# Performance work log

Measured on AMD Instinct MI355X. Metric: run time of the kernel, lower is better.

## Reference

```python
import jax, jax.numpy as jnp
import numpy as np


def _conv(x, w, b=None, stride=1, pad=0):
    y = jax.lax.conv_general_dilated(x, w, (stride, stride), [(pad, pad), (pad, pad)],
                                     dimension_numbers=('NCHW', 'OIHW', 'NCHW'))
    if b is not None:
        y = y + b[None, :, None, None]
    return y


def _slice3d(grid, guide):
    # Trilinear grid_sample, align_corners=False, zero padding.
    # grid: (N, C=12, D=8, GH, GW); guide: (N,1,H,W) in [-1,1]
    N, C, D, GH, GW = grid.shape
    H, W = guide.shape[2], guide.shape[3]
    xs = 2.0 * jnp.arange(W, dtype=grid.dtype) / max(W - 1, 1) - 1.0
    ys = 2.0 * jnp.arange(H, dtype=grid.dtype) / max(H - 1, 1) - 1.0
    gx = ((xs + 1.0) * GW - 1.0) * 0.5               # (W,)
    gy = ((ys + 1.0) * GH - 1.0) * 0.5               # (H,)
    gz = ((guide[:, 0] + 1.0) * D - 1.0) * 0.5       # (N,H,W)
    x0f = jnp.floor(gx); y0f = jnp.floor(gy); z0f = jnp.floor(gz)
    fx = gx - x0f; fy = gy - y0f; fz = gz - z0f
    x0 = x0f.astype(jnp.int32); y0 = y0f.astype(jnp.int32); z0 = z0f.astype(jnp.int32)
    gf = grid.reshape(N, C, D * GH * GW)

    def corner(zi, yi, xi, wz, wy, wx):
        mask = ((zi >= 0) & (zi < D)) & ((yi >= 0) & (yi < GH))[None, :, None] & ((xi >= 0) & (xi < GW))[None, None, :]
        zc = jnp.clip(zi, 0, D - 1); yc = jnp.clip(yi, 0, GH - 1); xc = jnp.clip(xi, 0, GW - 1)
        flat = zc * (GH * GW) + yc[None, :, None] * GW + xc[None, None, :]   # (N,H,W)
        v = jnp.take_along_axis(gf, flat.reshape(N, 1, H * W), axis=2).reshape(N, C, H, W)
        w = (wz * wy[None, :, None] * wx[None, None, :]) * mask.astype(grid.dtype)  # (N,H,W)
        return v * w[:, None]

    out = jnp.zeros((N, C, H, W), grid.dtype)
    for dz in (0, 1):
        for dy in (0, 1):
            for dx in (0, 1):
                out = out + corner(z0 + dz, y0 + dy, x0 + dx,
                                   fz if dz else 1.0 - fz,
                                   fy if dy else 1.0 - fy,
                                   fx if dx else 1.0 - fx)
    return out


def setup_inputs() -> dict:
    key = jax.random.key(0)
    ks = jax.random.split(key, 40)
    def w(i, shape):
        return jax.random.normal(ks[i], shape, jnp.float32) * 0.05
    return {
        'low_res': jax.random.uniform(ks[0], (4, 3, 256, 256), jnp.float32),
        'full_res': jax.random.uniform(ks[1], (4, 1, 1024, 1024), jnp.float32),
        'w0': w(2, (8, 3, 3, 3)), 'b0': w(3, (8,)),
        'w1': w(4, (16, 8, 3, 3)), 'b1': w(5, (16,)),
        'w2': w(6, (32, 16, 3, 3)), 'b2': w(7, (32,)),
        'w3': w(8, (64, 32, 3, 3)), 'b3': w(9, (64,)),
        'wl0': w(10, (64, 64, 3, 3)), 'bl0': w(11, (64,)),
        'wl1': w(12, (64, 64, 3, 3)),
        'wg1': w(13, (128, 64, 3, 3)), 'bg1': w(14, (128,)),
        'wg2': w(15, (256, 128, 3, 3)), 'bg2': w(16, (256,)),
        'wf1': w(17, (256, 448, 1, 1)), 'bf1': w(18, (256,)),
        'wf2': w(19, (128, 256, 1, 1)), 'bf2': w(20, (128,)),
        'wf3': w(21, (64, 128, 1, 1)), 'bf3': w(22, (64,)),
        'wlin': w(23, (96, 64, 1, 1)), 'blin': w(24, (96,)),
        'wgd1': w(25, (16, 1, 3, 3)), 'bgd1': w(26, (16,)),
        'wgd2': w(27, (1, 16, 1, 1)), 'bgd2': w(28, (1,)),
        'wau1': w(29, (16, 1, 1, 1)), 'bau1': w(30, (16,)),
        'wau2': w(31, (1, 16, 1, 1)), 'bau2': w(32, (1,)),
        'wav1': w(33, (16, 1, 1, 1)), 'bav1': w(34, (16,)),
        'wav2': w(35, (1, 16, 1, 1)), 'bav2': w(36, (1,)),
    }


def reference(low_res, full_res, w0, b0, w1, b1, w2, b2, w3, b3, wl0, bl0, wl1,
              wg1, bg1, wg2, bg2, wf1, bf1, wf2, bf2, wf3, bf3, wlin, blin,
              wgd1, bgd1, wgd2, bgd2, wau1, bau1, wau2, bau2, wav1, bav1, wav2, bav2):
    relu = jax.nn.relu
    N = low_res.shape[0]
    H, W = full_res.shape[2], full_res.shape[3]
    fake = jax.image.resize(low_res, (N, 3, H, W), 'bilinear')
    # splat stack: 4 stride-2 convs
    x = relu(_conv(low_res, w0, b0, 2, 1))
    x = relu(_conv(x, w1, b1, 2, 1))
    x = relu(_conv(x, w2, b2, 2, 1))
    splat = relu(_conv(x, w3, b3, 2, 1))                 # (N,64,16,16)
    local = _conv(relu(_conv(splat, wl0, bl0, 1, 1)), wl1, None, 1, 1)
    # global branch
    a0 = splat.mean(axis=(2, 3), keepdims=True)
    x1 = relu(_conv(splat, wg1, bg1, 2, 1))
    a1 = x1.mean(axis=(2, 3), keepdims=True)
    x2 = relu(_conv(x1, wg2, bg2, 2, 1))
    a2 = x2.mean(axis=(2, 3), keepdims=True)
    a = jnp.concatenate([a0, a1, a2], axis=1)            # (N,448,1,1)
    a = relu(_conv(a, wf1, bf1))
    a = relu(_conv(a, wf2, bf2))
    glob = relu(_conv(a, wf3, bf3))                      # (N,64,1,1)
    fused = relu(glob + local)
    fused = _conv(fused, wlin, blin)                     # (N,96,16,16)
    grid = fused.reshape(N, 12, 8, fused.shape[2], fused.shape[3])
    guidemap = jnp.tanh(_conv(relu(_conv(full_res, wgd1, bgd1, 1, 1)), wgd2, bgd2))
    coeff = _slice3d(grid, guidemap)                     # (N,12,H,W)
    Y = full_res * coeff[:, 3:4] + coeff[:, 0:3].sum(axis=1, keepdims=True)
    U0 = full_res * coeff[:, 7:8] + coeff[:, 4:7].sum(axis=1, keepdims=True)
    V0 = full_res * coeff[:, 11:12] + coeff[:, 8:11].sum(axis=1, keepdims=True)
    U = jnp.tanh(_conv(relu(_conv(U0, wau1, bau1)), wau2, bau2)) + fake[:, 1:2]
    V = jnp.tanh(_conv(relu(_conv(V0, wav1, bav1)), wav2, bav2)) + fake[:, 2:3]
    return jnp.concatenate([Y, U, V], axis=1)
```

## Files before the change

kernel.cpp:

```cpp
#include <hip/hip_runtime.h>
#include <math.h>


typedef float v2f __attribute__((ext_vector_type(2)));

__device__ __forceinline__ float tanh_fast(float x) {
    float e = __expf(2.0f * x);
    return 1.0f - 2.0f / (e + 1.0f);
}

template<int CIN, int COUT, int HIN, int WIN, int HOUT, int WOUT>
__global__ __launch_bounds__(256) void conv_s2_small(
    const float* __restrict__ in, const float* __restrict__ w,
    const float* __restrict__ b, float* __restrict__ out)
{
    int idx = blockIdx.x * 256 + threadIdx.x;
    int wo = idx % WOUT; int t = idx / WOUT;
    int ho = t % HOUT; t /= HOUT;
    int co = t % COUT; int n = t / COUT;
    float acc = b[co];
    int hi0 = ho * 2 - 1, wi0 = wo * 2 - 1;
    const float* wp = w + (size_t)co * CIN * 9;
    #pragma unroll
    for (int ci = 0; ci < CIN; ++ci) {
        const float* ip = in + ((size_t)(n * CIN + ci)) * HIN * WIN;
        const float* wc = wp + ci * 9;
        #pragma unroll
        for (int kh = 0; kh < 3; ++kh) {
            int hi = hi0 + kh;
            if ((unsigned)hi >= (unsigned)HIN) continue;
            const float* row = ip + hi * WIN;
            #pragma unroll
            for (int kw = 0; kw < 3; ++kw) {
                int wi = wi0 + kw;
                if ((unsigned)wi >= (unsigned)WIN) continue;
                acc = fmaf(wc[kh * 3 + kw], row[wi], acc);
            }
        }
    }
    out[idx] = fmaxf(acc, 0.0f);
}

template<int CIN, int PARTS, int STRIDE, bool RELU, bool HASB,
         int COUT, int HIN, int WIN, int HOUT, int WOUT>
__device__ __forceinline__ void conv_p_dev(
    const float* __restrict__ in, const float* __restrict__ w,
    const float* __restrict__ b, float* __restrict__ out,
    int tb, float* red)
{
    constexpr int CPT = CIN / PARTS;
    constexpr int OPB = 256 / PARTS;
    int part = threadIdx.x / OPB;
    int oidx = threadIdx.x % OPB;
    int o = tb * OPB + oidx;
    int wo = o % WOUT; int t = o / WOUT;
    int ho = t % HOUT; t /= HOUT;
    int co = t % COUT; int n = t / COUT;
    int hi0 = ho * STRIDE - 1, wi0 = wo * STRIDE - 1;
    const float* wp = w + ((size_t)co * CIN + part * CPT) * 9;
    const float* ip = in + ((size_t)n * CIN + part * CPT) * HIN * WIN;
    float acc = 0.0f;
    #pragma unroll
    for (int ci = 0; ci < CPT; ++ci) {
        const float* ic = ip + (size_t)ci * HIN * WIN;
        const float* wc = wp + ci * 9;
        #pragma unroll
        for (int kh = 0; kh < 3; ++kh) {
            int hi = hi0 + kh;
            if ((unsigned)hi >= (unsigned)HIN) continue;
            const float* row = ic + hi * WIN;
            #pragma unroll
            for (int kw = 0; kw < 3; ++kw) {
                int wi = wi0 + kw;
                if ((unsigned)wi >= (unsigned)WIN) continue;
                acc = fmaf(wc[kh * 3 + kw], row[wi], acc);
            }
        }
    }
    red[threadIdx.x] = acc;
    __syncthreads();
    if (part == 0) {
        float s = acc;
        #pragma unroll
        for (int p = 1; p < PARTS; ++p) s += red[p * OPB + oidx];
        if (HASB) s += b[co];
        if (RELU) s = fmaxf(s, 0.0f);
        out[o] = s;
    }
}

__global__ __launch_bounds__(256) void conv2_k(
    const float* __restrict__ in, const float* __restrict__ w,
    const float* __restrict__ b, float* __restrict__ out)
{
    __shared__ float red[256];
    conv_p_dev<16, 4, 2, true, true, 32, 64, 64, 32, 32>(in, w, b, out, blockIdx.x, red);
}

__global__ __launch_bounds__(256) void conv3_k(
    const float* __restrict__ in, const float* __restrict__ w,
    const float* __restrict__ b, float* __restrict__ out)
{
    __shared__ float red[256];
    conv_p_dev<32, 8, 2, true, true, 64, 32, 32, 16, 16>(in, w, b, out, blockIdx.x, red);
}

__global__ __launch_bounds__(256) void k5_l0_g1(
    const float* __restrict__ splat,
    const float* __restrict__ wl0, const float* __restrict__ bl0, float* __restrict__ l0o,
    const float* __restrict__ wg1, const float* __restrict__ bg1, float* __restrict__ x1)
{
    __shared__ float red[256];
    int bid = blockIdx.x;
    if (bid < 4096)
        conv_p_dev<64, 16, 1, true, true, 64, 16, 16, 16, 16>(splat, wl0, bl0, l0o, bid, red);
    else
        conv_p_dev<64, 16, 2, true, true, 128, 16, 16, 8, 8>(splat, wg1, bg1, x1, bid - 4096, red);
}

__global__ __launch_bounds__(256) void k6_l1_g2_means(
    const float* __restrict__ l0o, const float* __restrict__ wl1, float* __restrict__ localb,
    const float* __restrict__ x1, const float* __restrict__ wg2,
    const float* __restrict__ bg2, float* __restrict__ x2,
    const float* __restrict__ splat, float* __restrict__ avec)
{
    __shared__ float red[256];
    int bid = blockIdx.x;
    if (bid < 4096) {
        conv_p_dev<64, 16, 1, false, false, 64, 16, 16, 16, 16>(l0o, wl1, nullptr, localb, bid, red);
    } else if (bid < 5120) {
        conv_p_dev<128, 16, 2, true, true, 256, 8, 8, 4, 4>(x1, wg2, bg2, x2, bid - 4096, red);
    } else if (bid < 5184) {
        int wid = (bid - 5120) * 4 + (threadIdx.x >> 6);
        int lane = threadIdx.x & 63;
        int n = wid >> 6, c = wid & 63;
        const float* p = splat + ((size_t)(n * 64 + c)) * 256;
        float s = p[lane] + p[lane + 64] + p[lane + 128] + p[lane + 192];
        #pragma unroll
        for (int off = 32; off; off >>= 1) s += __shfl_down(s, off, 64);
        if (lane == 0) avec[n * 448 + c] = s * (1.0f / 256.0f);
    } else {
        int wid = (bid - 5184) * 4 + (threadIdx.x >> 6);
        int lane = threadIdx.x & 63;
        int n = wid >> 7, c = wid & 127;
        const float* p = x1 + ((size_t)(n * 128 + c)) * 64;
        float s = p[lane];
        #pragma unroll
        for (int off = 32; off; off >>= 1) s += __shfl_down(s, off, 64);
        if (lane == 0) avec[n * 448 + 64 + c] = s * (1.0f / 64.0f);
    }
}

__global__ __launch_bounds__(256) void fc_k(
    const float* __restrict__ avec, const float* __restrict__ x2,
    const float* __restrict__ wf1, const float* __restrict__ bf1,
    const float* __restrict__ wf2, const float* __restrict__ bf2,
    const float* __restrict__ wf3, const float* __restrict__ bf3,
    float* __restrict__ glob)
{
    __shared__ float a[448];
    __shared__ float h1[256];
    __shared__ float h2[128];
    int n = blockIdx.x, t = threadIdx.x;
    if (t < 192) a[t] = avec[n * 448 + t];
    {
        const float* p = x2 + ((size_t)(n * 256 + t)) * 16;
        float s = 0.0f;
        #pragma unroll
        for (int i = 0; i < 16; ++i) s += p[i];
        a[192 + t] = s * (1.0f / 16.0f);
    }
    __syncthreads();
    {
        float a0 = 0, a1 = 0, a2 = 0, a3 = 0;
        const float* wp = wf1 + (size_t)t * 448;
        for (int i = 0; i < 448; i += 4) {
            a0 = fmaf(wp[i], a[i], a0); a1 = fmaf(wp[i + 1], a[i + 1], a1);
            a2 = fmaf(wp[i + 2], a[i + 2], a2); a3 = fmaf(wp[i + 3], a[i + 3], a3);
        }
        float s = a0 + a1 + a2 + a3 + bf1[t];
        __syncthreads();
        h1[t] = fmaxf(s, 0.0f);
    }
    __syncthreads();
    if (t < 128) {
        float a0 = 0, a1 = 0, a2 = 0, a3 = 0;
        const float* wp = wf2 + (size_t)t * 256;
        for (int i = 0; i < 256; i += 4) {
            a0 = fmaf(wp[i], h1[i], a0); a1 = fmaf(wp[i + 1], h1[i + 1], a1);
            a2 = fmaf(wp[i + 2], h1[i + 2], a2); a3 = fmaf(wp[i + 3], h1[i + 3], a3);
        }
        h2[t] = fmaxf(a0 + a1 + a2 + a3 + bf2[t], 0.0f);
    }
    __syncthreads();
    if (t < 64) {
        float a0 = 0, a1 = 0, a2 = 0, a3 = 0;
        const float* wp = wf3 + (size_t)t * 128;
        for (int i = 0; i < 128; i += 4) {
            a0 = fmaf(wp[i], h2[i], a0); a1 = fmaf(wp[i + 1], h2[i + 1], a1);
            a2 = fmaf(wp[i + 2], h2[i + 2], a2); a3 = fmaf(wp[i + 3], h2[i + 3], a3);
        }
        glob[n * 64 + t] = fmaxf(a0 + a1 + a2 + a3 + bf3[t], 0.0f);
    }
}

__global__ __launch_bounds__(256) void fuse_grid(
    const float* __restrict__ glob, const float* __restrict__ local,
    const float* __restrict__ wlin, const float* __restrict__ blin,
    float* __restrict__ grid)
{
    int idx = blockIdx.x * 256 + threadIdx.x;
    int p = idx & 255; int k = (idx >> 8) % 96; int n = idx / (96 * 256);
    float acc = blin[k];
    const float* wp = wlin + k * 64;
    const float* gl = glob + n * 64;
    const float* lo = local + (size_t)n * 64 * 256 + p;
    #pragma unroll 8
    for (int c = 0; c < 64; ++c)
        acc = fmaf(wp[c], fmaxf(gl[c] + lo[c * 256], 0.0f), acc);
    int ch = k >> 3; int z = k & 7;
    grid[(((size_t)(n * 8 + z)) * 256 + p) * 12 + ch] = acc;
}

__global__ __launch_bounds__(256) void hdr_out_v3(
    const float* __restrict__ full, const float* __restrict__ low,
    const float* __restrict__ grid,
    const float* __restrict__ wgd1, const float* __restrict__ bgd1,
    const float* __restrict__ wgd2, const float* __restrict__ bgd2,
    const float* __restrict__ wau1, const float* __restrict__ bau1,
    const float* __restrict__ wau2, const float* __restrict__ bau2,
    const float* __restrict__ wav1, const float* __restrict__ bav1,
    const float* __restrict__ wav2, const float* __restrict__ bav2,
    float* __restrict__ out)
{
    int tid = blockIdx.x * 256 + threadIdx.x;
    int x0 = (tid & 255) << 2;
    int y = (tid >> 8) & 1023;
    int n = tid >> 18;
    const float* fp = full + ((size_t)n << 20);

    float v[3][6];
    #pragma unroll
    for (int r = 0; r < 3; ++r) {
        int yy = y + r - 1;
        bool okr = (unsigned)yy < 1024u;
        const float* row = fp + (size_t)yy * 1024;
        if (okr) {
            float4 m = *(const float4*)(row + x0);
            v[r][1] = m.x; v[r][2] = m.y; v[r][3] = m.z; v[r][4] = m.w;
            v[r][0] = (x0 > 0) ? row[x0 - 1] : 0.0f;
            v[r][5] = (x0 < 1020) ? row[x0 + 4] : 0.0f;
        } else {
            #pragma unroll
            for (int j = 0; j < 6; ++j) v[r][j] = 0.0f;
        }
    }

    float gacc[4];
    float bb = bgd2[0];
    #pragma unroll
    for (int px = 0; px < 4; ++px) gacc[px] = bb;
    #pragma unroll
    for (int k = 0; k < 16; ++k) {
        const float* wk = wgd1 + k * 9;
        float q0 = wk[0], q1 = wk[1], q2 = wk[2];
        float q3 = wk[3], q4 = wk[4], q5 = wk[5];
        float q6 = wk[6], q7 = wk[7], q8 = wk[8];
        float bk = bgd1[k], wo = wgd2[k];
        #pragma unroll
        for (int px = 0; px < 4; ++px) {
            float h = bk;
            h = fmaf(q0, v[0][px], h); h = fmaf(q1, v[0][px + 1], h); h = fmaf(q2, v[0][px + 2], h);
            h = fmaf(q3, v[1][px], h); h = fmaf(q4, v[1][px + 1], h); h = fmaf(q5, v[1][px + 2], h);
            h = fmaf(q6, v[2][px], h); h = fmaf(q7, v[2][px + 1], h); h = fmaf(q8, v[2][px + 2], h);
            gacc[px] = fmaf(wo, fmaxf(h, 0.0f), gacc[px]);
        }
    }

    float gyc = (y * (32.0f / 1023.0f) - 1.0f) * 0.5f;
    float y0f = floorf(gyc); float fy = gyc - y0f; int iy = (int)y0f;
    float wy0 = (iy >= 0 && iy < 16) ? (1.0f - fy) : 0.0f;
    float wy1 = (iy + 1 < 16) ? fy : 0.0f;
    int yi0 = min(max(iy, 0), 15), yi1 = min(iy + 1, 15);

    float sy = (y + 0.5f) * 0.25f - 0.5f;
    float syf = floorf(sy); float fyl = sy - syf;
    int jy0 = max((int)syf, 0), jy1 = min((int)syf + 1, 255);
    int jc = x0 >> 2;
    int c0 = max(jc - 1, 0), c2 = min(jc + 1, 255);
    const float* lr1 = low + ((size_t)(n * 3 + 1)) * 65536;
    const float* lr2 = low + ((size_t)(n * 3 + 2)) * 65536;
    float ua = lr1[jy0 * 256 + c0] + fyl * (lr1[jy1 * 256 + c0] - lr1[jy0 * 256 + c0]);
    float ub = lr1[jy0 * 256 + jc] + fyl * (lr1[jy1 * 256 + jc] - lr1[jy0 * 256 + jc]);
    float uc = lr1[jy0 * 256 + c2] + fyl * (lr1[jy1 * 256 + c2] - lr1[jy0 * 256 + c2]);
    float va = lr2[jy0 * 256 + c0] + fyl * (lr2[jy1 * 256 + c0] - lr2[jy0 * 256 + c0]);
    float vb = lr2[jy0 * 256 + jc] + fyl * (lr2[jy1 * 256 + jc] - lr2[jy0 * 256 + jc]);
    float vc = lr2[jy0 * 256 + c2] + fyl * (lr2[jy1 * 256 + c2] - lr2[jy0 * 256 + c2]);
    const float cfx[4] = {0.625f, 0.875f, 0.125f, 0.375f};

    const float* gbase = grid + (size_t)n * 24576;
    float Yo[4], Uo[4], Vo[4];

    #pragma unroll
    for (int px = 0; px < 4; ++px) {
        int x = x0 + px;
        float g = tanh_fast(gacc[px]);

        float gxc = (x * (32.0f / 1023.0f) - 1.0f) * 0.5f;
        float gzc = 4.0f * g + 3.5f;
        float x0f = floorf(gxc), z0f = floorf(gzc);
        float fx = gxc - x0f, fz = gzc - z0f;
        int ix = (int)x0f, iz = (int)z0f;

        float wx0 = (ix >= 0 && ix < 16) ? (1.0f - fx) : 0.0f;
        float wx1 = (ix + 1 < 16) ? fx : 0.0f;
        float wz0 = (iz >= 0 && iz < 8) ? (1.0f - fz) : 0.0f;
        float wz1 = (iz + 1 >= 0 && iz + 1 < 8) ? fz : 0.0f;
        int xi0 = min(max(ix, 0), 15), xi1 = min(ix + 1, 15);
        int zi0 = min(max(iz, 0), 7),  zi1 = min(max(iz + 1, 0), 7);

        float w00 = wy0 * wx0, w01 = wy0 * wx1, w10 = wy1 * wx0, w11 = wy1 * wx1;
        int o00 = yi0 * 16 + xi0, o01 = yi0 * 16 + xi1;
        int o10 = yi1 * 16 + xi0, o11 = yi1 * 16 + xi1;
        int z0b = zi0 * 256, z1b = zi1 * 256;

        v2f a01 = {0.f, 0.f}, a23 = {0.f, 0.f}, a45 = {0.f, 0.f};
        v2f a67 = {0.f, 0.f}, a89 = {0.f, 0.f}, aAB = {0.f, 0.f};

        #define CORNER(OFF, WK) { \
            const v2f* q = (const v2f*)(gbase + (size_t)(OFF) * 12); \
            float wk_ = (WK); v2f wv = {wk_, wk_}; \
            a01 += wv * q[0]; a23 += wv * q[1]; a45 += wv * q[2]; \
            a67 += wv * q[3]; a89 += wv * q[4]; aAB += wv * q[5]; }

        CORNER(z0b + o00, wz0 * w00)
        CORNER(z0b + o01, wz0 * w01)
        CORNER(z0b + o10, wz0 * w10)
        CORNER(z0b + o11, wz0 * w11)
        CORNER(z1b + o00, wz1 * w00)
        CORNER(z1b + o01, wz1 * w01)
        CORNER(z1b + o10, wz1 * w10)
        CORNER(z1b + o11, wz1 * w11)
        #undef CORNER

        float p = v[1][px + 1];
        float Yv = fmaf(p, a23.y, a01.x + a01.y + a23.x);
        float U0 = fmaf(p, a67.y, a45.x + a45.y + a67.x);
        float V0 = fmaf(p, aAB.y, a89.x + a89.y + aAB.x);

        v2f uv = {U0, V0};
        v2f acc2 = {bau2[0], bav2[0]};
        #pragma unroll
        for (int k = 0; k < 16; ++k) {
            v2f w1k = {wau1[k], wav1[k]};
            v2f b1k = {bau1[k], bav1[k]};
            v2f w2k = {wau2[k], wav2[k]};
            v2f h = w1k * uv + b1k;
            h.x = fmaxf(h.x, 0.0f); h.y = fmaxf(h.y, 0.0f);
            acc2 += w2k * h;
        }

        float f1 = (px < 2) ? (ua + cfx[px] * (ub - ua)) : (ub + cfx[px] * (uc - ub));
        float f2 = (px < 2) ? (va + cfx[px] * (vb - va)) : (vb + cfx[px] * (vc - vb));

        Yo[px] = Yv;
        Uo[px] = tanh_fast(acc2.x) + f1;
        Vo[px] = tanh_fast(acc2.y) + f2;
    }

    size_t base = ((size_t)n * 3) * 1048576 + (size_t)y * 1024 + x0;
    *(float4*)(out + base)            = make_float4(Yo[0], Yo[1], Yo[2], Yo[3]);
    *(float4*)(out + base + 1048576)  = make_float4(Uo[0], Uo[1], Uo[2], Uo[3]);
    *(float4*)(out + base + 2097152)  = make_float4(Vo[0], Vo[1], Vo[2], Vo[3]);
}

extern "C" void kernel_launch(void* const* d_in, const int* in_sizes, int n_in,
                              void* d_out, int out_size, void* d_ws, size_t ws_size,
                              hipStream_t stream)
{
    const float* low  = (const float*)d_in[0];
    const float* full = (const float*)d_in[1];
    const float* w0 = (const float*)d_in[2];  const float* b0 = (const float*)d_in[3];
    const float* w1 = (const float*)d_in[4];  const float* b1 = (const float*)d_in[5];
    const float* w2 = (const float*)d_in[6];  const float* b2 = (const float*)d_in[7];
    const float* w3 = (const float*)d_in[8];  const float* b3 = (const float*)d_in[9];
    const float* wl0 = (const float*)d_in[10]; const float* bl0 = (const float*)d_in[11];
    const float* wl1 = (const float*)d_in[12];
    const float* wg1 = (const float*)d_in[13]; const float* bg1 = (const float*)d_in[14];
    const float* wg2 = (const float*)d_in[15]; const float* bg2 = (const float*)d_in[16];
    const float* wf1 = (const float*)d_in[17]; const float* bf1 = (const float*)d_in[18];
    const float* wf2 = (const float*)d_in[19]; const float* bf2 = (const float*)d_in[20];
    const float* wf3 = (const float*)d_in[21]; const float* bf3 = (const float*)d_in[22];
    const float* wlin = (const float*)d_in[23]; const float* blin = (const float*)d_in[24];
    const float* wgd1 = (const float*)d_in[25]; const float* bgd1 = (const float*)d_in[26];
    const float* wgd2 = (const float*)d_in[27]; const float* bgd2 = (const float*)d_in[28];
    const float* wau1 = (const float*)d_in[29]; const float* bau1 = (const float*)d_in[30];
    const float* wau2 = (const float*)d_in[31]; const float* bau2 = (const float*)d_in[32];
    const float* wav1 = (const float*)d_in[33]; const float* bav1 = (const float*)d_in[34];
    const float* wav2 = (const float*)d_in[35]; const float* bav2 = (const float*)d_in[36];
    float* out = (float*)d_out;

    float* ws = (float*)d_ws;
    float* t0b    = ws;
    float* t1b    = t0b + 524288;
    float* t2b    = t1b + 262144;
    float* splat  = t2b + 131072;
    float* l0o    = splat + 65536;
    float* localb = l0o + 65536;
    float* x1b    = localb + 65536;
    float* x2b    = x1b + 32768;
    float* avec   = x2b + 16384;
    float* glob   = avec + 1792;
    float* gridb  = glob + 256;

    conv_s2_small<3, 8, 256, 256, 128, 128><<<2048, 256, 0, stream>>>(low, w0, b0, t0b);
    conv_s2_small<8, 16, 128, 128, 64, 64><<<1024, 256, 0, stream>>>(t0b, w1, b1, t1b);
    conv2_k<<<2048, 256, 0, stream>>>(t1b, w2, b2, t2b);
    conv3_k<<<2048, 256, 0, stream>>>(t2b, w3, b3, splat);
    k5_l0_g1<<<6144, 256, 0, stream>>>(splat, wl0, bl0, l0o, wg1, bg1, x1b);
    k6_l1_g2_means<<<5312, 256, 0, stream>>>(l0o, wl1, localb, x1b, wg2, bg2, x2b, splat, avec);
    fc_k<<<4, 256, 0, stream>>>(avec, x2b, wf1, bf1, wf2, bf2, wf3, bf3, glob);
    fuse_grid<<<384, 256, 0, stream>>>(glob, localb, wlin, blin, gridb);
    hdr_out_v3<<<4096, 256, 0, stream>>>(full, low, gridb,
        wgd1, bgd1, wgd2, bgd2, wau1, bau1, wau2, bau2, wav1, bav1, wav2, bav2, out);
}
```

Baseline: 395.0 us.

## Fuse conv pairs via LDS tiles, merge FC with grid fusion, revert hdr kernel

```diff
diff --git a/kernel.cpp b/kernel.cpp
--- a/kernel.cpp
+++ b/kernel.cpp
@@ -1,44 +1,147 @@
 #include <hip/hip_runtime.h>
 #include <math.h>
 
-
-typedef float v2f __attribute__((ext_vector_type(2)));
 
 __device__ __forceinline__ float tanh_fast(float x) {
     float e = __expf(2.0f * x);
     return 1.0f - 2.0f / (e + 1.0f);
 }
 
-template<int CIN, int COUT, int HIN, int WIN, int HOUT, int WOUT>
-__global__ __launch_bounds__(256) void conv_s2_small(
-    const float* __restrict__ in, const float* __restrict__ w,
-    const float* __restrict__ b, float* __restrict__ out)
-{
-    int idx = blockIdx.x * 256 + threadIdx.x;
-    int wo = idx % WOUT; int t = idx / WOUT;
-    int ho = t % HOUT; t /= HOUT;
-    int co = t % COUT; int n = t / COUT;
-    float acc = b[co];
-    int hi0 = ho * 2 - 1, wi0 = wo * 2 - 1;
-    const float* wp = w + (size_t)co * CIN * 9;
-    #pragma unroll
-    for (int ci = 0; ci < CIN; ++ci) {
-        const float* ip = in + ((size_t)(n * CIN + ci)) * HIN * WIN;
-        const float* wc = wp + ci * 9;
+__global__ __launch_bounds__(256) void k01_fused(
+    const float* __restrict__ low,
+    const float* __restrict__ w0, const float* __restrict__ b0,
+    const float* __restrict__ w1, const float* __restrict__ b1,
+    float* __restrict__ t1out)
+{
+    __shared__ float t0L[8 * 33 * 33];
+    int blk = blockIdx.x;
+    int n = blk >> 4; int tile = blk & 15;
+    int R0 = (tile >> 2) * 16, C0 = (tile & 3) * 16;
+    const float* lowN = low + (size_t)n * 3 * 65536;
+
+    for (int t = threadIdx.x; t < 8712; t += 256) {
+        int ch = t / 1089; int rem = t % 1089;
+        int r = rem / 33; int cc = rem % 33;
+        int gy = 2 * R0 - 1 + r, gx = 2 * C0 - 1 + cc;
+        float val = 0.0f;
+        if ((unsigned)gy < 128u && (unsigned)gx < 128u) {
+            float acc = b0[ch];
+            const float* wp = w0 + ch * 27;
+            int hi0 = 2 * gy - 1, wi0 = 2 * gx - 1;
+            #pragma unroll
+            for (int ci = 0; ci < 3; ++ci) {
+                const float* ip = lowN + (size_t)ci * 65536;
+                #pragma unroll
+                for (int kh = 0; kh < 3; ++kh) {
+                    int hi = hi0 + kh;
+                    if ((unsigned)hi >= 256u) continue;
+                    #pragma unroll
+                    for (int kw = 0; kw < 3; ++kw) {
+                        int wi = wi0 + kw;
+                        if ((unsigned)wi >= 256u) continue;
+                        acc = fmaf(wp[ci * 9 + kh * 3 + kw], ip[hi * 256 + wi], acc);
+                    }
+                }
+            }
+            val = fmaxf(acc, 0.0f);
+        }
+        t0L[t] = val;
+    }
+    __syncthreads();
+
+    int c = threadIdx.x >> 4, i = threadIdx.x & 15;
+    float acc[16];
+    float bc = b1[c];
+    #pragma unroll
+    for (int j = 0; j < 16; ++j) acc[j] = bc;
+    const float* wb = w1 + c * 72;
+    #pragma unroll
+    for (int ch = 0; ch < 8; ++ch) {
         #pragma unroll
         for (int kh = 0; kh < 3; ++kh) {
-            int hi = hi0 + kh;
-            if ((unsigned)hi >= (unsigned)HIN) continue;
-            const float* row = ip + hi * WIN;
-            #pragma unroll
-            for (int kw = 0; kw < 3; ++kw) {
-                int wi = wi0 + kw;
-                if ((unsigned)wi >= (unsigned)WIN) continue;
-                acc = fmaf(wc[kh * 3 + kw], row[wi], acc);
+            const float* rowp = &t0L[ch * 1089 + (2 * i + kh) * 33];
+            float q0 = wb[ch * 9 + kh * 3 + 0];
+            float q1 = wb[ch * 9 + kh * 3 + 1];
+            float q2 = wb[ch * 9 + kh * 3 + 2];
+            #pragma unroll
+            for (int j = 0; j < 16; ++j) {
+                acc[j] = fmaf(q0, rowp[2 * j], acc[j]);
+                acc[j] = fmaf(q1, rowp[2 * j + 1], acc[j]);
+                acc[j] = fmaf(q2, rowp[2 * j + 2], acc[j]);
             }
         }
     }
-    out[idx] = fmaxf(acc, 0.0f);
+    float* op = t1out + (((size_t)(n * 16 + c)) * 64 + (R0 + i)) * 64 + C0;
+    #pragma unroll
+    for (int j = 0; j < 16; ++j) op[j] = fmaxf(acc[j], 0.0f);
+}
+
+__global__ __launch_bounds__(256) void k23_fused(
+    const float* __restrict__ t1, const float* __restrict__ w2,
+    const float* __restrict__ b2, const float* __restrict__ w3,
+    const float* __restrict__ b3, float* __restrict__ splat)
+{
+    __shared__ float t2L[32 * 81];
+    int blk = blockIdx.x;
+    int n = blk >> 4; int tile = blk & 15;
+    int R0 = (tile >> 2) * 4, C0 = (tile & 3) * 4;
+    const float* t1N = t1 + (size_t)n * 16 * 4096;
+
+    for (int t = threadIdx.x; t < 2592; t += 256) {
+        int ch = t / 81; int rem = t % 81;
+        int r = rem / 9; int cc = rem % 9;
+        int gy = 2 * R0 - 1 + r, gx = 2 * C0 - 1 + cc;
+        float val = 0.0f;
+        if ((unsigned)gy < 32u && (unsigned)gx < 32u) {
+            float acc = b2[ch];
+            const float* wp = w2 + ch * 144;
+            int hi0 = 2 * gy - 1, wi0 = 2 * gx - 1;
+            #pragma unroll
+            for (int ci = 0; ci < 16; ++ci) {
+                const float* ip = t1N + (size_t)ci * 4096;
+                #pragma unroll
+                for (int kh = 0; kh < 3; ++kh) {
+                    int hi = hi0 + kh;
+                    if ((unsigned)hi >= 64u) continue;
+                    #pragma unroll
+                    for (int kw = 0; kw < 3; ++kw) {
+                        int wi = wi0 + kw;
+                        if ((unsigned)wi >= 64u) continue;
+                        acc = fmaf(wp[ci * 9 + kh * 3 + kw], ip[hi * 64 + wi], acc);
+                    }
+                }
+            }
+            val = fmaxf(acc, 0.0f);
+        }
+        t2L[t] = val;
+    }
+    __syncthreads();
+
+    int c = threadIdx.x >> 2, i = threadIdx.x & 3;
+    float acc[4];
+    float bc = b3[c];
+    #pragma unroll
+    for (int j = 0; j < 4; ++j) acc[j] = bc;
+    const float* wb = w3 + c * 288;
+    #pragma unroll
+    for (int ch = 0; ch < 32; ++ch) {
+        #pragma unroll
+        for (int kh = 0; kh < 3; ++kh) {
+            const float* rowp = &t2L[ch * 81 + (2 * i + kh) * 9];
+            float q0 = wb[ch * 9 + kh * 3 + 0];
+            float q1 = wb[ch * 9 + kh * 3 + 1];
+            float q2 = wb[ch * 9 + kh * 3 + 2];
+            #pragma unroll
+            for (int j = 0; j < 4; ++j) {
+                acc[j] = fmaf(q0, rowp[2 * j], acc[j]);
+                acc[j] = fmaf(q1, rowp[2 * j + 1], acc[j]);
+                acc[j] = fmaf(q2, rowp[2 * j + 2], acc[j]);
+            }
+        }
+    }
+    float* op = splat + (((size_t)(n * 64 + c)) * 16 + (R0 + i)) * 16 + C0;
+    #pragma unroll
+    for (int j = 0; j < 4; ++j) op[j] = fmaxf(acc[j], 0.0f);
 }
 
 template<int CIN, int PARTS, int STRIDE, bool RELU, bool HASB,
@@ -89,40 +192,35 @@
     }
 }
 
-__global__ __launch_bounds__(256) void conv2_k(
-    const float* __restrict__ in, const float* __restrict__ w,
-    const float* __restrict__ b, float* __restrict__ out)
-{
-    __shared__ float red[256];
-    conv_p_dev<16, 4, 2, true, true, 32, 64, 64, 32, 32>(in, w, b, out, blockIdx.x, red);
-}
-
-__global__ __launch_bounds__(256) void conv3_k(
-    const float* __restrict__ in, const float* __restrict__ w,
-    const float* __restrict__ b, float* __restrict__ out)
-{
-    __shared__ float red[256];
-    conv_p_dev<32, 8, 2, true, true, 64, 32, 32, 16, 16>(in, w, b, out, blockIdx.x, red);
-}
-
-__global__ __launch_bounds__(256) void k5_l0_g1(
+__global__ __launch_bounds__(256) void k5_l0_g1_means(
     const float* __restrict__ splat,
     const float* __restrict__ wl0, const float* __restrict__ bl0, float* __restrict__ l0o,
-    const float* __restrict__ wg1, const float* __restrict__ bg1, float* __restrict__ x1)
+    const float* __restrict__ wg1, const float* __restrict__ bg1, float* __restrict__ x1,
+    float* __restrict__ avec)
 {
     __shared__ float red[256];
     int bid = blockIdx.x;
-    if (bid < 4096)
+    if (bid < 4096) {
         conv_p_dev<64, 16, 1, true, true, 64, 16, 16, 16, 16>(splat, wl0, bl0, l0o, bid, red);
-    else
+    } else if (bid < 6144) {
         conv_p_dev<64, 16, 2, true, true, 128, 16, 16, 8, 8>(splat, wg1, bg1, x1, bid - 4096, red);
+    } else {
+        int wid = (bid - 6144) * 4 + (threadIdx.x >> 6);
+        int lane = threadIdx.x & 63;
+        int n = wid >> 6, c = wid & 63;
+        const float* p = splat + ((size_t)(n * 64 + c)) * 256;
+        float s = p[lane] + p[lane + 64] + p[lane + 128] + p[lane + 192];
+        #pragma unroll
+        for (int off = 32; off; off >>= 1) s += __shfl_down(s, off, 64);
+        if (lane == 0) avec[n * 448 + c] = s * (1.0f / 256.0f);
+    }
 }
 
 __global__ __launch_bounds__(256) void k6_l1_g2_means(
     const float* __restrict__ l0o, const float* __restrict__ wl1, float* __restrict__ localb,
     const float* __restrict__ x1, const float* __restrict__ wg2,
     const float* __restrict__ bg2, float* __restrict__ x2,
-    const float* __restrict__ splat, float* __restrict__ avec)
+    float* __restrict__ avec)
 {
     __shared__ float red[256];
     int bid = blockIdx.x;
@@ -130,17 +228,8 @@
         conv_p_dev<64, 16, 1, false, false, 64, 16, 16, 16, 16>(l0o, wl1, nullptr, localb, bid, red);
     } else if (bid < 5120) {
         conv_p_dev<128, 16, 2, true, true, 256, 8, 8, 4, 4>(x1, wg2, bg2, x2, bid - 4096, red);
-    } else if (bid < 5184) {
+    } else {
         int wid = (bid - 5120) * 4 + (threadIdx.x >> 6);
-        int lane = threadIdx.x & 63;
-        int n = wid >> 6, c = wid & 63;
-        const float* p = splat + ((size_t)(n * 64 + c)) * 256;
-        float s = p[lane] + p[lane + 64] + p[lane + 128] + p[lane + 192];
-        #pragma unroll
-        for (int off = 32; off; off >>= 1) s += __shfl_down(s, off, 64);
-        if (lane == 0) avec[n * 448 + c] = s * (1.0f / 256.0f);
-    } else {
-        int wid = (bid - 5184) * 4 + (threadIdx.x >> 6);
         int lane = threadIdx.x & 63;
         int n = wid >> 7, c = wid & 127;
         const float* p = x1 + ((size_t)(n * 128 + c)) * 64;
@@ -151,17 +240,20 @@
     }
 }
 
-__global__ __launch_bounds__(256) void fc_k(
+__global__ __launch_bounds__(256) void kfc_fuse(
     const float* __restrict__ avec, const float* __restrict__ x2,
     const float* __restrict__ wf1, const float* __restrict__ bf1,
     const float* __restrict__ wf2, const float* __restrict__ bf2,
     const float* __restrict__ wf3, const float* __restrict__ bf3,
-    float* __restrict__ glob)
+    const float* __restrict__ local,
+    const float* __restrict__ wlin, const float* __restrict__ blin,
+    float* __restrict__ grid)
 {
     __shared__ float a[448];
     __shared__ float h1[256];
     __shared__ float h2[128];
-    int n = blockIdx.x, t = threadIdx.x;
+    __shared__ float gl[64];
+    int n = blockIdx.x / 96; int k = blockIdx.x % 96; int t = threadIdx.x;
     if (t < 192) a[t] = avec[n * 448 + t];
     {
         const float* p = x2 + ((size_t)(n * 256 + t)) * 16;
@@ -178,9 +270,7 @@
             a0 = fmaf(wp[i], a[i], a0); a1 = fmaf(wp[i + 1], a[i + 1], a1);
             a2 = fmaf(wp[i + 2], a[i + 2], a2); a3 = fmaf(wp[i + 3], a[i + 3], a3);
         }
-        float s = a0 + a1 + a2 + a3 + bf1[t];
-        __syncthreads();
-        h1[t] = fmaxf(s, 0.0f);
+        h1[t] = fmaxf(a0 + a1 + a2 + a3 + bf1[t], 0.0f);
     }
     __syncthreads();
     if (t < 128) {
@@ -200,29 +290,20 @@
             a0 = fmaf(wp[i], h2[i], a0); a1 = fmaf(wp[i + 1], h2[i + 1], a1);
             a2 = fmaf(wp[i + 2], h2[i + 2], a2); a3 = fmaf(wp[i + 3], h2[i + 3], a3);
         }
-        glob[n * 64 + t] = fmaxf(a0 + a1 + a2 + a3 + bf3[t], 0.0f);
-    }
-}
-
-__global__ __launch_bounds__(256) void fuse_grid(
-    const float* __restrict__ glob, const float* __restrict__ local,
-    const float* __restrict__ wlin, const float* __restrict__ blin,
-    float* __restrict__ grid)
-{
-    int idx = blockIdx.x * 256 + threadIdx.x;
-    int p = idx & 255; int k = (idx >> 8) % 96; int n = idx / (96 * 256);
+        gl[t] = fmaxf(a0 + a1 + a2 + a3 + bf3[t], 0.0f);
+    }
+    __syncthreads();
     float acc = blin[k];
     const float* wp = wlin + k * 64;
-    const float* gl = glob + n * 64;
-    const float* lo = local + (size_t)n * 64 * 256 + p;
+    const float* lo = local + (size_t)n * 64 * 256 + t;
     #pragma unroll 8
     for (int c = 0; c < 64; ++c)
         acc = fmaf(wp[c], fmaxf(gl[c] + lo[c * 256], 0.0f), acc);
     int ch = k >> 3; int z = k & 7;
-    grid[(((size_t)(n * 8 + z)) * 256 + p) * 12 + ch] = acc;
-}
-
-__global__ __launch_bounds__(256) void hdr_out_v3(
+    grid[(((size_t)(n * 8 + z)) * 256 + t) * 12 + ch] = acc;
+}
+
+__global__ __launch_bounds__(256, 4) void hdr_out_v2(
     const float* __restrict__ full, const float* __restrict__ low,
     const float* __restrict__ grid,
     const float* __restrict__ wgd1, const float* __restrict__ bgd1,
@@ -277,27 +358,6 @@
         }
     }
 
-    float gyc = (y * (32.0f / 1023.0f) - 1.0f) * 0.5f;
-    float y0f = floorf(gyc); float fy = gyc - y0f; int iy = (int)y0f;
-    float wy0 = (iy >= 0 && iy < 16) ? (1.0f - fy) : 0.0f;
-    float wy1 = (iy + 1 < 16) ? fy : 0.0f;
-    int yi0 = min(max(iy, 0), 15), yi1 = min(iy + 1, 15);
-
-    float sy = (y + 0.5f) * 0.25f - 0.5f;
-    float syf = floorf(sy); float fyl = sy - syf;
-    int jy0 = max((int)syf, 0), jy1 = min((int)syf + 1, 255);
-    int jc = x0 >> 2;
-    int c0 = max(jc - 1, 0), c2 = min(jc + 1, 255);
-    const float* lr1 = low + ((size_t)(n * 3 + 1)) * 65536;
-    const float* lr2 = low + ((size_t)(n * 3 + 2)) * 65536;
-    float ua = lr1[jy0 * 256 + c0] + fyl * (lr1[jy1 * 256 + c0] - lr1[jy0 * 256 + c0]);
-    float ub = lr1[jy0 * 256 + jc] + fyl * (lr1[jy1 * 256 + jc] - lr1[jy0 * 256 + jc]);
-    float uc = lr1[jy0 * 256 + c2] + fyl * (lr1[jy1 * 256 + c2] - lr1[jy0 * 256 + c2]);
-    float va = lr2[jy0 * 256 + c0] + fyl * (lr2[jy1 * 256 + c0] - lr2[jy0 * 256 + c0]);
-    float vb = lr2[jy0 * 256 + jc] + fyl * (lr2[jy1 * 256 + jc] - lr2[jy0 * 256 + jc]);
-    float vc = lr2[jy0 * 256 + c2] + fyl * (lr2[jy1 * 256 + c2] - lr2[jy0 * 256 + c2]);
-    const float cfx[4] = {0.625f, 0.875f, 0.125f, 0.375f};
-
     const float* gbase = grid + (size_t)n * 24576;
     float Yo[4], Uo[4], Vo[4];
 
@@ -307,16 +367,20 @@
         float g = tanh_fast(gacc[px]);
 
         float gxc = (x * (32.0f / 1023.0f) - 1.0f) * 0.5f;
+        float gyc = (y * (32.0f / 1023.0f) - 1.0f) * 0.5f;
         float gzc = 4.0f * g + 3.5f;
-        float x0f = floorf(gxc), z0f = floorf(gzc);
-        float fx = gxc - x0f, fz = gzc - z0f;
-        int ix = (int)x0f, iz = (int)z0f;
+        float x0f = floorf(gxc), y0f = floorf(gyc), z0f = floorf(gzc);
+        float fx = gxc - x0f, fy = gyc - y0f, fz = gzc - z0f;
+        int ix = (int)x0f, iy = (int)y0f, iz = (int)z0f;
 
         float wx0 = (ix >= 0 && ix < 16) ? (1.0f - fx) : 0.0f;
         float wx1 = (ix + 1 < 16) ? fx : 0.0f;
+        float wy0 = (iy >= 0 && iy < 16) ? (1.0f - fy) : 0.0f;
+        float wy1 = (iy + 1 < 16) ? fy : 0.0f;
         float wz0 = (iz >= 0 && iz < 8) ? (1.0f - fz) : 0.0f;
         float wz1 = (iz + 1 >= 0 && iz + 1 < 8) ? fz : 0.0f;
         int xi0 = min(max(ix, 0), 15), xi1 = min(ix + 1, 15);
+        int yi0 = min(max(iy, 0), 15), yi1 = min(iy + 1, 15);
         int zi0 = min(max(iz, 0), 7),  zi1 = min(max(iz + 1, 0), 7);
 
         float w00 = wy0 * wx0, w01 = wy0 * wx1, w10 = wy1 * wx0, w11 = wy1 * wx1;
@@ -324,14 +388,20 @@
         int o10 = yi1 * 16 + xi0, o11 = yi1 * 16 + xi1;
         int z0b = zi0 * 256, z1b = zi1 * 256;
 
-        v2f a01 = {0.f, 0.f}, a23 = {0.f, 0.f}, a45 = {0.f, 0.f};
-        v2f a67 = {0.f, 0.f}, a89 = {0.f, 0.f}, aAB = {0.f, 0.f};
+        float acc[12];
+        #pragma unroll
+        for (int i = 0; i < 12; ++i) acc[i] = 0.0f;
 
         #define CORNER(OFF, WK) { \
-            const v2f* q = (const v2f*)(gbase + (size_t)(OFF) * 12); \
-            float wk_ = (WK); v2f wv = {wk_, wk_}; \
-            a01 += wv * q[0]; a23 += wv * q[1]; a45 += wv * q[2]; \
-            a67 += wv * q[3]; a89 += wv * q[4]; aAB += wv * q[5]; }
+            const float4* q = (const float4*)(gbase + (size_t)(OFF) * 12); \
+            float wk_ = (WK); \
+            float4 A = q[0], B = q[1], C = q[2]; \
+            acc[0] = fmaf(wk_, A.x, acc[0]); acc[1] = fmaf(wk_, A.y, acc[1]); \
+            acc[2] = fmaf(wk_, A.z, acc[2]); acc[3] = fmaf(wk_, A.w, acc[3]); \
+            acc[4] = fmaf(wk_, B.x, acc[4]); acc[5] = fmaf(wk_, B.y, acc[5]); \
+            acc[6] = fmaf(wk_, B.z, acc[6]); acc[7] = fmaf(wk_, B.w, acc[7]); \
+            acc[8] = fmaf(wk_, C.x, acc[8]); acc[9] = fmaf(wk_, C.y, acc[9]); \
+            acc[10] = fmaf(wk_, C.z, acc[10]); acc[11] = fmaf(wk_, C.w, acc[11]); }
 
         CORNER(z0b + o00, wz0 * w00)
         CORNER(z0b + o01, wz0 * w01)
@@ -344,28 +414,35 @@
         #undef CORNER
 
         float p = v[1][px + 1];
-        float Yv = fmaf(p, a23.y, a01.x + a01.y + a23.x);
-        float U0 = fmaf(p, a67.y, a45.x + a45.y + a67.x);
-        float V0 = fmaf(p, aAB.y, a89.x + a89.y + aAB.x);
-
-        v2f uv = {U0, V0};
-        v2f acc2 = {bau2[0], bav2[0]};
-        #pragma unroll
-        for (int k = 0; k < 16; ++k) {
-            v2f w1k = {wau1[k], wav1[k]};
-            v2f b1k = {bau1[k], bav1[k]};
-            v2f w2k = {wau2[k], wav2[k]};
-            v2f h = w1k * uv + b1k;
-            h.x = fmaxf(h.x, 0.0f); h.y = fmaxf(h.y, 0.0f);
-            acc2 += w2k * h;
-        }
-
-        float f1 = (px < 2) ? (ua + cfx[px] * (ub - ua)) : (ub + cfx[px] * (uc - ub));
-        float f2 = (px < 2) ? (va + cfx[px] * (vb - va)) : (vb + cfx[px] * (vc - vb));
+        float Yv = fmaf(p, acc[3],  acc[0] + acc[1] + acc[2]);
+        float U0 = fmaf(p, acc[7],  acc[4] + acc[5] + acc[6]);
+        float V0 = fmaf(p, acc[11], acc[8] + acc[9] + acc[10]);
+
+        float uacc = bau2[0];
+        #pragma unroll
+        for (int k = 0; k < 16; ++k)
+            uacc = fmaf(wau2[k], fmaxf(fmaf(wau1[k], U0, bau1[k]), 0.0f), uacc);
+        float vacc = bav2[0];
+        #pragma unroll
+        for (int k = 0; k < 16; ++k)
+            vacc = fmaf(wav2[k], fmaxf(fmaf(wav1[k], V0, bav1[k]), 0.0f), vacc);
+
+        float sx = (x + 0.5f) * 0.25f - 0.5f;
+        float sy = (y + 0.5f) * 0.25f - 0.5f;
+        float sxf = floorf(sx), syf = floorf(sy);
+        float fxl = sx - sxf, fyl = sy - syf;
+        int jx0 = max((int)sxf, 0), jx1 = min((int)sxf + 1, 255);
+        int jy0 = max((int)syf, 0), jy1 = min((int)syf + 1, 255);
+        const float* lr1 = low + ((size_t)(n * 3 + 1)) * 65536;
+        const float* lr2 = low + ((size_t)(n * 3 + 2)) * 65536;
+        float f1 = (1.0f - fyl) * ((1.0f - fxl) * lr1[jy0 * 256 + jx0] + fxl * lr1[jy0 * 256 + jx1])
+                 + fyl * ((1.0f - fxl) * lr1[jy1 * 256 + jx0] + fxl * lr1[jy1 * 256 + jx1]);
+        float f2 = (1.0f - fyl) * ((1.0f - fxl) * lr2[jy0 * 256 + jx0] + fxl * lr2[jy0 * 256 + jx1])
+                 + fyl * ((1.0f - fxl) * lr2[jy1 * 256 + jx0] + fxl * lr2[jy1 * 256 + jx1]);
 
         Yo[px] = Yv;
-        Uo[px] = tanh_fast(acc2.x) + f1;
-        Vo[px] = tanh_fast(acc2.y) + f2;
+        Uo[px] = tanh_fast(uacc) + f1;
+        Vo[px] = tanh_fast(vacc) + f2;
     }
 
     size_t base = ((size_t)n * 3) * 1048576 + (size_t)y * 1024 + x0;
@@ -401,26 +478,21 @@
     float* out = (float*)d_out;
 
     float* ws = (float*)d_ws;
-    float* t0b    = ws;
-    float* t1b    = t0b + 524288;
-    float* t2b    = t1b + 262144;
-    float* splat  = t2b + 131072;
+    float* t1b    = ws;
+    float* splat  = t1b + 262144;
     float* l0o    = splat + 65536;
     float* localb = l0o + 65536;
     float* x1b    = localb + 65536;
     float* x2b    = x1b + 32768;
     float* avec   = x2b + 16384;
-    float* glob   = avec + 1792;
-    float* gridb  = glob + 256;
-
-    conv_s2_small<3, 8, 256, 256, 128, 128><<<2048, 256, 0, stream>>>(low, w0, b0, t0b);
-    conv_s2_small<8, 16, 128, 128, 64, 64><<<1024, 256, 0, stream>>>(t0b, w1, b1, t1b);
-    conv2_k<<<2048, 256, 0, stream>>>(t1b, w2, b2, t2b);
-    conv3_k<<<2048, 256, 0, stream>>>(t2b, w3, b3, splat);
-    k5_l0_g1<<<6144, 256, 0, stream>>>(splat, wl0, bl0, l0o, wg1, bg1, x1b);
-    k6_l1_g2_means<<<5312, 256, 0, stream>>>(l0o, wl1, localb, x1b, wg2, bg2, x2b, splat, avec);
-    fc_k<<<4, 256, 0, stream>>>(avec, x2b, wf1, bf1, wf2, bf2, wf3, bf3, glob);
-    fuse_grid<<<384, 256, 0, stream>>>(glob, localb, wlin, blin, gridb);
-    hdr_out_v3<<<4096, 256, 0, stream>>>(full, low, gridb,
+    float* gridb  = avec + 1792;
+
+    k01_fused<<<64, 256, 0, stream>>>(low, w0, b0, w1, b1, t1b);
+    k23_fused<<<64, 256, 0, stream>>>(t1b, w2, b2, w3, b3, splat);
+    k5_l0_g1_means<<<6208, 256, 0, stream>>>(splat, wl0, bl0, l0o, wg1, bg1, x1b, avec);
+    k6_l1_g2_means<<<5248, 256, 0, stream>>>(l0o, wl1, localb, x1b, wg2, bg2, x2b, avec);
+    kfc_fuse<<<384, 256, 0, stream>>>(avec, x2b, wf1, bf1, wf2, bf2, wf3, bf3,
+                                      localb, wlin, blin, gridb);
+    hdr_out_v2<<<4096, 256, 0, stream>>>(full, low, gridb,
         wgd1, bgd1, wgd2, bgd2, wau1, bau1, wau2, bau2, wav1, bav1, wav2, bav2, out);
 }
```

Result: slower. 600.7 us (+52.1%).
